# Kernel optimization log

Hardware: AMD Instinct MI355X
Metric: run time of the kernel (lower is better)

## Reference

```python
import jax, jax.numpy as jnp
import numpy as np

L, B, T, D, H, A, F, V, BIAS_DIM, E = 6, 16, 512, 512, 8, 64, 2048, 10000, 4, 200000
LN_EPS = 1e-3  # keras LayerNormalization default


def positional_encoding(d, max_len):
    pos = np.arange(max_len, dtype=np.float32)[:, None]
    i = np.arange(d, dtype=np.float32)[None, :]
    angle = pos / np.power(10000.0, (2.0 * np.floor(i / 2.0)) / d)
    pe = np.where((np.arange(d) % 2) == 0, np.sin(angle), np.cos(angle))
    return jnp.asarray(pe, jnp.float32)


def layer_norm(x, g, b):
    mu = jnp.mean(x, -1, keepdims=True)
    var = jnp.mean(jnp.square(x - mu), -1, keepdims=True)
    return (x - mu) * jax.lax.rsqrt(var + LN_EPS) * g + b


def attention(x, masks, bias_idx, Wq, Wk, Wv, Wo, be, bs):
    q = jnp.einsum('btd,dha->btha', x, Wq)
    k = jnp.einsum('btd,dha->btha', x, Wk)
    v = jnp.einsum('btd,dha->btha', x, Wv)
    alpha = jnp.einsum('bkha,bqha->bhqk', k, q)
    # sparse edge bias: scalar per edge = bias_embs[type] @ bias_scalar
    ev = (be[bias_idx[:, 0]] @ bs)[:, 0]                      # [E]
    dense = jnp.zeros((x.shape[0], x.shape[1], x.shape[1]), x.dtype)
    dense = dense.at[bias_idx[:, 1], bias_idx[:, 2], bias_idx[:, 3]].add(ev)  # scatter_nd semantics (add)
    ksum = jnp.sum(k, -1)                                     # [B,T,H]
    alpha = alpha + jnp.einsum('bqk,bkh->bhqk', dense, ksum)
    alpha = alpha * jax.lax.rsqrt(jnp.float32(A))
    alpha = alpha * masks + (1.0 - jnp.ceil(masks)) * jnp.finfo(jnp.float32).min
    alpha = jax.nn.softmax(alpha, -1)
    ctx = jnp.einsum('bhqk,bkha->bqha', alpha, v)
    return jnp.einsum('btha,had->btd', ctx, Wo)


def setup_inputs() -> dict:
    key = jax.random.key(0)
    ks = jax.random.split(key, 24)
    tokens = jax.random.randint(ks[0], (B, T), 0, V, dtype=jnp.int32)
    masks = jnp.ones((B, 1, T, T), jnp.float32)
    ab = jnp.stack([
        jax.random.randint(ks[1], (E,), 0, BIAS_DIM, dtype=jnp.int32),
        jax.random.randint(ks[2], (E,), 0, B, dtype=jnp.int32),
        jax.random.randint(ks[3], (E,), 0, T, dtype=jnp.int32),
        jax.random.randint(ks[4], (E,), 0, T, dtype=jnp.int32)], axis=1)
    s = 0.03
    return {
        'tokens': tokens, 'masks': masks, 'attention_bias': ab,
        'embed': jax.random.normal(ks[5], (V, D)) * (D ** -0.5),
        'Wq': jax.random.normal(ks[6], (L, D, H, A)) * s,
        'Wk': jax.random.normal(ks[7], (L, D, H, A)) * s,
        'Wv': jax.random.normal(ks[8], (L, D, H, A)) * s,
        'Wo': jax.random.normal(ks[9], (L, H, A, D)) * s,
        'be': jax.random.normal(ks[10], (L, BIAS_DIM, A)) * s,
        'bs': jax.random.normal(ks[11], (L, A, 1)) * s,
        'ln_g': jnp.ones((L, 2, D)), 'ln_b': jnp.zeros((L, 2, D)),
        'ff1_w': jax.random.normal(ks[12], (L, D, F)) * s,
        'ff1_b': jnp.zeros((L, F)),
        'ff2_w': jax.random.normal(ks[13], (L, F, D)) * s,
        'ff2_b': jnp.zeros((L, D)),
        'lnout_g': jnp.ones((D,)), 'lnout_b': jnp.zeros((D,)),
    }


def reference(tokens, masks, attention_bias, embed, Wq, Wk, Wv, Wo, be, bs,
              ln_g, ln_b, ff1_w, ff1_b, ff2_w, ff2_b, lnout_g, lnout_b):
    pos_enc = positional_encoding(D, 5000)
    x = embed[tokens] * jnp.sqrt(jnp.float32(D)) + pos_enc[:T]
    for l in range(L):
        h = layer_norm(x, ln_g[l, 0], ln_b[l, 0])
        x = x + attention(h, masks, attention_bias, Wq[l], Wk[l], Wv[l], Wo[l], be[l], bs[l])
        h = layer_norm(x, ln_g[l, 1], ln_b[l, 1])
        x = x + jax.nn.relu(h @ ff1_w[l] + ff1_b[l]) @ ff2_w[l] + ff2_b[l]
    return layer_norm(x, lnout_g, lnout_b)
```

## Files before the change

kernel.cpp:

```cpp
#include <hip/hip_runtime.h>
#include <hip/hip_bf16.h>

#define LNUM 6
#define BB 16
#define TT 512
#define DD 512
#define HH 8
#define AA 64
#define FFD 2048
#define EE 200000
#define BIASDIM 4
#define ATT_NEG (-3.402823466e38f)

typedef __bf16 bf16_t;
typedef __attribute__((ext_vector_type(8))) __bf16 bf16x8;
typedef __attribute__((ext_vector_type(4))) float f32x4;

typedef __attribute__((address_space(3))) void lds_void;
typedef const __attribute__((address_space(1))) void glb_void;

__device__ __forceinline__ void async_load16(const bf16_t* g, bf16_t* l) {
    __builtin_amdgcn_global_load_lds((glb_void*)g, (lds_void*)l, 16, 0, 0);
}

__global__ __launch_bounds__(256) void embed_pe_kernel(
    const int* __restrict__ tokens, const float* __restrict__ embed,
    float* __restrict__ x)
{
    int idx = blockIdx.x * 256 + threadIdx.x;
    int d  = idx & (DD - 1);
    int bt = idx >> 9;
    int t  = bt & (TT - 1);
    int tok = tokens[bt];
    float e = embed[(long long)tok * DD + d] * 22.62741699796952f;
    float p = (float)(2 * (d >> 1)) * (1.0f / (float)DD);
    float denom = exp2f(p * 13.287712379549449f);
    float angle = (float)t / denom;
    float pe = (d & 1) ? cosf(angle) : sinf(angle);
    x[idx] = e + pe;
}

template <typename TO>
__global__ __launch_bounds__(256) void ln_kernel(
    const float* __restrict__ x, TO* __restrict__ y,
    const float* __restrict__ g, const float* __restrict__ b)
{
    long long row = blockIdx.x;
    const float* xr = x + row * DD;
    int tid = threadIdx.x;
    float v0 = xr[tid], v1 = xr[tid + 256];
    float s = v0 + v1, sq = v0 * v0 + v1 * v1;
#pragma unroll
    for (int o = 32; o > 0; o >>= 1) {
        s  += __shfl_down(s, o);
        sq += __shfl_down(sq, o);
    }
    __shared__ float ss[4], sq4[4];
    if ((tid & 63) == 0) { ss[tid >> 6] = s; sq4[tid >> 6] = sq; }
    __syncthreads();
    float st  = ss[0] + ss[1] + ss[2] + ss[3];
    float sqt = sq4[0] + sq4[1] + sq4[2] + sq4[3];
    float mean = st * (1.0f / DD);
    float var  = sqt * (1.0f / DD) - mean * mean;
    float inv  = rsqrtf(var + 1e-3f);
    y[row * DD + tid]       = (TO)((v0 - mean) * inv * g[tid]       + b[tid]);
    y[row * DD + tid + 256] = (TO)((v1 - mean) * inv * g[tid + 256] + b[tid + 256]);
}

template <typename TO, int S>
__global__ __launch_bounds__(256) void reduce_ln_kernel(
    float* __restrict__ x, const float* __restrict__ P,
    TO* __restrict__ y, const float* __restrict__ g, const float* __restrict__ b)
{
    const long long NXc = (long long)BB * TT * DD;
    long long row = blockIdx.x;
    int tid = threadIdx.x;
    long long i0 = row * DD + tid;
    float v0 = x[i0], v1 = x[i0 + 256];
#pragma unroll
    for (int s = 0; s < S; s++) {
        v0 += P[(long long)s * NXc + i0];
        v1 += P[(long long)s * NXc + i0 + 256];
    }
    x[i0] = v0; x[i0 + 256] = v1;
    float s2 = v0 + v1, sq = v0 * v0 + v1 * v1;
#pragma unroll
    for (int o = 32; o > 0; o >>= 1) {
        s2 += __shfl_down(s2, o);
        sq += __shfl_down(sq, o);
    }
    __shared__ float ss[4], sq4[4];
    if ((tid & 63) == 0) { ss[tid >> 6] = s2; sq4[tid >> 6] = sq; }
    __syncthreads();
    float st  = ss[0] + ss[1] + ss[2] + ss[3];
    float sqt = sq4[0] + sq4[1] + sq4[2] + sq4[3];
    float mean = st * (1.0f / DD);
    float var  = sqt * (1.0f / DD) - mean * mean;
    float inv  = rsqrtf(var + 1e-3f);
    y[i0]       = (TO)((v0 - mean) * inv * g[tid]       + b[tid]);
    y[i0 + 256] = (TO)((v1 - mean) * inv * g[tid + 256] + b[tid + 256]);
}

__global__ __launch_bounds__(256) void ksum_kernel(
    const bf16_t* __restrict__ k, float* __restrict__ ks)
{
    int idx = blockIdx.x * 256 + threadIdx.x;
    long long base = (long long)idx * AA;
    float s = 0.f;
#pragma unroll
    for (int a = 0; a < AA; a++) s += (float)k[base + a];
    ks[idx] = s;
}

__global__ __launch_bounds__(256) void cnt_scatter_kernel(
    const int* __restrict__ ab, unsigned int* __restrict__ cm)
{
    int e = blockIdx.x * 256 + threadIdx.x;
    if (e < EE) {
        int ty = ab[e * 4 + 0];
        int b  = ab[e * 4 + 1];
        int q  = ab[e * 4 + 2];
        int kk = ab[e * 4 + 3];
        atomicAdd(&cm[((long long)b * TT + q) * TT + kk], 1u << (4 * ty));
    }
}

__global__ __launch_bounds__(256) void cm_mask_kernel(
    unsigned int* __restrict__ cm, const float* __restrict__ masks)
{
    long long i = ((long long)blockIdx.x * 256 + threadIdx.x) * 4;
    uint4 c = *(const uint4*)(cm + i);
    f32x4 m = *(const f32x4*)(masks + i);
    c.x = (__float_as_uint(m[0]) & 0xffff0000u) | (c.x & 0xffffu);
    c.y = (__float_as_uint(m[1]) & 0xffff0000u) | (c.y & 0xffffu);
    c.z = (__float_as_uint(m[2]) & 0xffff0000u) | (c.z & 0xffffu);
    c.w = (__float_as_uint(m[3]) & 0xffff0000u) | (c.w & 0xffffu);
    *(uint4*)(cm + i) = c;
}

__global__ __launch_bounds__(256) void wconv_kernel(
    const float* __restrict__ in, bf16_t* __restrict__ out, int R, int Cc)
{
    __shared__ bf16_t tile[64][65];
    int c0 = blockIdx.x * 64, r0 = blockIdx.y * 64;
    int tid = threadIdx.x;
#pragma unroll
    for (int i = 0; i < 16; i++) {
        int idx = tid + i * 256; int r = idx >> 6, c = idx & 63;
        tile[c][r] = (bf16_t)in[(long long)(r0 + r) * Cc + c0 + c];
    }
    __syncthreads();
#pragma unroll
    for (int i = 0; i < 16; i++) {
        int idx = tid + i * 256; int rr = idx >> 6, cc = idx & 63;
        out[(long long)(c0 + rr) * R + r0 + cc] = tile[rr][cc];
    }
}

struct Ptr4 { const float* p[4]; };

__global__ __launch_bounds__(256) void wconv4_kernel(Ptr4 srcs, bf16_t* __restrict__ out)
{
    __shared__ bf16_t tile[64][65];
    int z = blockIdx.z;
    const float* in = srcs.p[z];
    bf16_t* o = out + (long long)z * DD * DD;
    int c0 = blockIdx.x * 64, r0 = blockIdx.y * 64;
    int tid = threadIdx.x;
#pragma unroll
    for (int i = 0; i < 16; i++) {
        int idx = tid + i * 256; int r = idx >> 6, c = idx & 63;
        tile[c][r] = (bf16_t)in[(long long)(r0 + r) * DD + c0 + c];
    }
    __syncthreads();
#pragma unroll
    for (int i = 0; i < 16; i++) {
        int idx = tid + i * 256; int rr = idx >> 6, cc = idx & 63;
        o[(long long)(c0 + rr) * DD + r0 + cc] = tile[rr][cc];
    }
}

__global__ __launch_bounds__(256) void vtrans_kernel(
    const bf16_t* __restrict__ v, bf16_t* __restrict__ vT)
{
    __shared__ bf16_t tile[64][65];
    int bh = blockIdx.y; int b = bh >> 3, h = bh & 7;
    int t0 = blockIdx.x * 64;
    int tid = threadIdx.x;
#pragma unroll
    for (int i = 0; i < 16; i++) {
        int idx = tid + i * 256; int r = idx >> 6, c = idx & 63;
        tile[c][r] = v[((long long)(b * TT + t0 + r) * HH + h) * AA + c];
    }
    __syncthreads();
#pragma unroll
    for (int i = 0; i < 16; i++) {
        int idx = tid + i * 256; int a = idx >> 6, t2 = idx & 63;
        vT[(((long long)b * HH + h) * AA + a) * TT + t0 + t2] = tile[a][t2];
    }
}

__global__ __launch_bounds__(256) void fused_attn_kernel(
    const bf16_t* __restrict__ qg, const bf16_t* __restrict__ kg,
    const bf16_t* __restrict__ vT, const unsigned int* __restrict__ cm,
    const float* __restrict__ ksum, const float* __restrict__ be_l,
    const float* __restrict__ bs_l, bf16_t* __restrict__ ctx)
{
    __shared__ __align__(16) bf16_t Ks[64 * 64];
    __shared__ __align__(16) bf16_t Vs[64 * 64];
    __shared__ __align__(16) bf16_t Plds[4 * 16 * 88];
    __shared__ float evs[BIASDIM];

    int tid = threadIdx.x;
    int wave = tid >> 6, lane = tid & 63;
    int row16 = lane & 15, quad = lane >> 4;
    int bid = blockIdx.x;
    int bh = bid & 127; int b = bh >> 3, h = bh & 7;
    int qw = (bid >> 7) * 64 + wave * 16;

    if (wave == 0) {
        float bsv = bs_l[lane];
#pragma unroll
        for (int t = 0; t < BIASDIM; t++) {
            float p = be_l[t * AA + lane] * bsv;
#pragma unroll
            for (int off = 32; off > 0; off >>= 1) p += __shfl_xor(p, off);
            if (lane == 0) evs[t] = p;
        }
    }

    bf16x8 qf[2];
    {
        const bf16_t* qp = qg + (((long long)b * TT + qw + row16) * HH + h) * AA + quad * 8;
        qf[0] = *(const bf16x8*)(qp);
        qf[1] = *(const bf16x8*)(qp + 32);
    }

    f32x4 o[4] = {};
    float m_r[4], l_r[4];
#pragma unroll
    for (int r = 0; r < 4; r++) { m_r[r] = -3.0e38f; l_r[r] = 0.f; }

    bf16_t* Pw = Plds + wave * 16 * 88;
    const unsigned int* cmbase = cm + (long long)b * TT * TT;
    const float* ksbase = ksum + (long long)b * TT * HH + h;

    for (int kt = 0; kt < 8; kt++) {
        int t0 = kt * 64;

        unsigned int cmw[4][4];
        float ksv4[4];
#pragma unroll
        for (int n = 0; n < 4; n++) {
            int ktok = t0 + n * 16 + row16;
            ksv4[n] = ksbase[(long long)ktok * HH];
#pragma unroll
            for (int r = 0; r < 4; r++)
                cmw[n][r] = cmbase[(long long)(qw + quad * 4 + r) * TT + ktok];
        }

#pragma unroll
        for (int p = tid; p < 512; p += 256) {
            int r = p >> 3, s = p & 7, c = s ^ (r & 7);
            async_load16(kg + (((long long)b * TT + t0 + r) * HH + h) * AA + c * 8,
                         Ks + p * 8);
        }
#pragma unroll
        for (int p = tid; p < 512; p += 256) {
            int r = p >> 3, s = p & 7, c = s ^ (r & 7);
            async_load16(vT + ((long long)bh * AA + r) * TT + t0 + c * 8,
                         Vs + p * 8);
        }
        __syncthreads();

        f32x4 s4[4] = {};
        __builtin_amdgcn_s_setprio(1);
#pragma unroll
        for (int n = 0; n < 4; n++) {
            int row = n * 16 + row16;
            int sw = row & 7;
            bf16x8 kf0 = *(const bf16x8*)(Ks + row * 64 + ((quad ^ sw) * 8));
            bf16x8 kf1 = *(const bf16x8*)(Ks + row * 64 + (((quad + 4) ^ sw) * 8));
            s4[n] = __builtin_amdgcn_mfma_f32_16x16x32_bf16(qf[0], kf0, s4[n], 0, 0, 0);
            s4[n] = __builtin_amdgcn_mfma_f32_16x16x32_bf16(qf[1], kf1, s4[n], 0, 0, 0);
        }
        __builtin_amdgcn_s_setprio(0);

        float e0 = evs[0], e1 = evs[1], e2 = evs[2], e3 = evs[3];
        float val[4][4];
#pragma unroll
        for (int n = 0; n < 4; n++) {
#pragma unroll
            for (int r = 0; r < 4; r++) {
                unsigned int w = cmw[n][r];
                float mk = __uint_as_float(w & 0xffff0000u);
                float d = e0 * (float)(w & 15u)
                        + e1 * (float)((w >> 4) & 15u)
                        + e2 * (float)((w >> 8) & 15u)
                        + e3 * (float)((w >> 12) & 15u);
                float vv = 0.125f * fmaf(d, ksv4[n], s4[n][r]);
                val[n][r] = (mk == 0.f) ? ATT_NEG : vv * mk;
            }
        }

        float scl[4];
#pragma unroll
        for (int r = 0; r < 4; r++) {
            float mx = fmaxf(fmaxf(val[0][r], val[1][r]), fmaxf(val[2][r], val[3][r]));
#pragma unroll
            for (int off = 1; off < 16; off <<= 1) mx = fmaxf(mx, __shfl_xor(mx, off));
            float mnew = fmaxf(m_r[r], mx);
            float sc = __expf(m_r[r] - mnew);
            float ps = 0.f;
#pragma unroll
            for (int n = 0; n < 4; n++) {
                float p = __expf(val[n][r] - mnew);
                val[n][r] = p;
                ps += p;
            }
#pragma unroll
            for (int off = 1; off < 16; off <<= 1) ps += __shfl_xor(ps, off);
            l_r[r] = l_r[r] * sc + ps;
            m_r[r] = mnew;
            scl[r] = sc;
        }
#pragma unroll
        for (int j = 0; j < 4; j++)
#pragma unroll
            for (int r = 0; r < 4; r++) o[j][r] *= scl[r];

#pragma unroll
        for (int n = 0; n < 4; n++)
#pragma unroll
            for (int r = 0; r < 4; r++)
                Pw[(quad * 4 + r) * 88 + n * 16 + row16] = (bf16_t)val[n][r];
        asm volatile("s_waitcnt lgkmcnt(0)" ::: "memory");

        bf16x8 pa0 = *(const bf16x8*)(Pw + row16 * 88 + quad * 8);
        bf16x8 pa1 = *(const bf16x8*)(Pw + row16 * 88 + 32 + quad * 8);
        __builtin_amdgcn_s_setprio(1);
#pragma unroll
        for (int j = 0; j < 4; j++) {
            int row = j * 16 + row16;
            int sw = row & 7;
            bf16x8 vb0 = *(const bf16x8*)(Vs + row * 64 + ((quad ^ sw) * 8));
            bf16x8 vb1 = *(const bf16x8*)(Vs + row * 64 + (((quad + 4) ^ sw) * 8));
            o[j] = __builtin_amdgcn_mfma_f32_16x16x32_bf16(pa0, vb0, o[j], 0, 0, 0);
            o[j] = __builtin_amdgcn_mfma_f32_16x16x32_bf16(pa1, vb1, o[j], 0, 0, 0);
        }
        __builtin_amdgcn_s_setprio(0);
        __syncthreads();
    }

#pragma unroll
    for (int r = 0; r < 4; r++) {
        float invl = 1.0f / l_r[r];
        int qgl = qw + quad * 4 + r;
        bf16_t* cp = ctx + (((long long)b * TT + qgl) * HH + h) * AA;
#pragma unroll
        for (int j = 0; j < 4; j++)
            cp[j * 16 + row16] = (bf16_t)(o[j][r] * invl);
    }
}

#define PSTAGE(kc0, slot)                                                     \
    {                                                                         \
        bf16_t* At = sm + (slot) * 16384;                                     \
        bf16_t* Bt = At + 8192;                                               \
        _Pragma("unroll")                                                     \
        for (int i = 0; i < 4; i++) {                                         \
            int qq = tid + i * 256;                                           \
            int r = qq >> 3, ck = qq & 7;                                     \
            int cc = (kc0) + ((ck ^ (r & 7)) * 8);                            \
            async_load16(Ag + (long long)(m0 + r) * lda + cc, At + qq * 8);   \
            async_load16(Bg + (long long)(n0 + r) * ldb + cc, Bt + qq * 8);   \
        }                                                                     \
    }

#define PLOAD()                                                               \
    _Pragma("unroll")                                                         \
    for (int mf = 0; mf < 4; mf++) {                                          \
        int ra = wm * 64 + mf * 16 + row16;                                   \
        _Pragma("unroll")                                                     \
        for (int ks2 = 0; ks2 < 2; ks2++)                                     \
            a8[mf][ks2] = *(const bf16x8*)(Ac + ra * 64 +                     \
                              (((ks2 * 4 + quad) ^ (ra & 7)) * 8));           \
    }                                                                         \
    _Pragma("unroll")                                                         \
    for (int nf = 0; nf < 4; nf++) {                                          \
        int rb = wn * 64 + nf * 16 + row16;                                   \
        _Pragma("unroll")                                                     \
        for (int ks2 = 0; ks2 < 2; ks2++)                                     \
            b8[nf][ks2] = *(const bf16x8*)(Bc + rb * 64 +                     \
                              (((ks2 * 4 + quad) ^ (rb & 7)) * 8));           \
    }

#define PMM()                                                                 \
    _Pragma("unroll")                                                         \
    for (int mf = 0; mf < 4; mf++)                                            \
        _Pragma("unroll")                                                     \
        for (int nf = 0; nf < 4; nf++)                                        \
            _Pragma("unroll")                                                 \
            for (int ks2 = 0; ks2 < 2; ks2++)                                 \
                acc[mf][nf] = __builtin_amdgcn_mfma_f32_16x16x32_bf16(        \
                    a8[mf][ks2], b8[nf][ks2], acc[mf][nf], 0, 0, 0);

#define PIPE_BODY(KBEG, NT)                                                   \
    PSTAGE((KBEG), 0);                                                        \
    int c = 0;                                                                \
    for (int t = 0; t < (NT); ++t, c ^= 1) {                                  \
        if (t + 1 < (NT)) {                                                   \
            PSTAGE((KBEG) + (t + 1) * 64, c ^ 1);                             \
            asm volatile("s_waitcnt vmcnt(8)" ::: "memory");                  \
        } else {                                                              \
            asm volatile("s_waitcnt vmcnt(0)" ::: "memory");                  \
        }                                                                     \
        __builtin_amdgcn_sched_barrier(0);                                    \
        __builtin_amdgcn_s_barrier();                                         \
        __builtin_amdgcn_sched_barrier(0);                                    \
        const bf16_t* Ac = sm + c * 16384;                                    \
        const bf16_t* Bc = Ac + 8192;                                         \
        bf16x8 a8[4][2], b8[4][2];                                            \
        PLOAD();                                                              \
        asm volatile("s_waitcnt lgkmcnt(0)" ::: "memory");                    \
        __builtin_amdgcn_sched_barrier(0);                                    \
        __builtin_amdgcn_s_barrier();                                        \
        __builtin_amdgcn_sched_barrier(0);                                    \
        __builtin_amdgcn_s_setprio(1);                                        \
        PMM();                                                                \
        __builtin_amdgcn_s_setprio(0);                                        \
    }

template <typename TC, int ACCUM, int RELU>
__global__ __launch_bounds__(256, 2) void gemm_pipe(
    const bf16_t* __restrict__ Ag, const bf16_t* __restrict__ Bg, TC* __restrict__ Cg,
    int K, int lda, int ldb, int ldc,
    long long sAz, long long sBz, long long sCz,
    const float* __restrict__ bias)
{
    extern __shared__ __align__(16) bf16_t sm[];
    int z = blockIdx.z;
    Ag += z * sAz; Bg += z * sBz; Cg += z * sCz;

    int tid = threadIdx.x;
    int wave = tid >> 6, lane = tid & 63;
    int wm = wave >> 1, wn = wave & 1;
    int row16 = lane & 15, quad = lane >> 4;
    int m0 = blockIdx.x * 128, n0 = blockIdx.y * 128;

    f32x4 acc[4][4] = {};
    int nt = K >> 6;
    PIPE_BODY(0, nt);

#pragma unroll
    for (int mf = 0; mf < 4; mf++) {
#pragma unroll
        for (int nf = 0; nf < 4; nf++) {
#pragma unroll
            for (int r = 0; r < 4; r++) {
                int m = m0 + wm * 64 + mf * 16 + quad * 4 + r;
                int n = n0 + wn * 64 + nf * 16 + row16;
                float vv = acc[mf][nf][r];
                if (bias) vv += bias[n];
                if (ACCUM) vv += (float)Cg[(long long)m * ldc + n];
                if (RELU) vv = fmaxf(vv, 0.f);
                Cg[(long long)m * ldc + n] = (TC)vv;
            }
        }
    }
}

template <int SPLIT>
__global__ __launch_bounds__(256, 2) void gemm_pipe_splitk(
    const bf16_t* __restrict__ Ag, const bf16_t* __restrict__ Bg,
    float* __restrict__ Cg, float* __restrict__ Pg,
    int K, int lda, int ldb, int ldc, const float* __restrict__ bias)
{
    extern __shared__ __align__(16) bf16_t sm[];
    int z = blockIdx.z;
    int kbeg = z * (K / SPLIT);

    int tid = threadIdx.x;
    int wave = tid >> 6, lane = tid & 63;
    int wm = wave >> 1, wn = wave & 1;
    int row16 = lane & 15, quad = lane >> 4;
    int m0 = blockIdx.x * 128, n0 = blockIdx.y * 128;

    f32x4 acc[4][4] = {};
    int nt = (K / SPLIT) >> 6;
    PIPE_BODY(kbeg, nt);

    const long long NXc = (long long)BB * TT * DD;
#pragma unroll
    for (int mf = 0; mf < 4; mf++) {
#pragma unroll
        for (int nf = 0; nf < 4; nf++) {
#pragma unroll
            for (int r = 0; r < 4; r++) {
                int m = m0 + wm * 64 + mf * 16 + quad * 4 + r;
                int n = n0 + wn * 64 + nf * 16 + row16;
                float vv = acc[mf][nf][r];
                long long ci = (long long)m * ldc + n;
                if (z == 0) {
                    if (bias) vv += bias[n];
                    Cg[ci] = Cg[ci] + vv;
                } else {
                    Pg[(long long)(z - 1) * NXc + ci] = vv;
                }
            }
        }
    }
}

extern "C" void kernel_launch(void* const* d_in, const int* in_sizes, int n_in,
                              void* d_out, int out_size, void* d_ws, size_t ws_size,
                              hipStream_t stream)
{
    const int*   tokens = (const int*)d_in[0];
    const float* masks  = (const float*)d_in[1];
    const int*   ab     = (const int*)d_in[2];
    const float* embed  = (const float*)d_in[3];
    const float* Wq     = (const float*)d_in[4];
    const float* Wk     = (const float*)d_in[5];
    const float* Wv     = (const float*)d_in[6];
    const float* Wo     = (const float*)d_in[7];
    const float* be     = (const float*)d_in[8];
    const float* bs     = (const float*)d_in[9];
    const float* ln_g   = (const float*)d_in[10];
    const float* ln_b   = (const float*)d_in[11];
    const float* ff1w   = (const float*)d_in[12];
    const float* ff1b   = (const float*)d_in[13];
    const float* ff2w   = (const float*)d_in[14];
    const float* ff2b   = (const float*)d_in[15];
    const float* lng    = (const float*)d_in[16];
    const float* lnb    = (const float*)d_in[17];
    float* out = (float*)d_out;

    const long long NX = (long long)BB * TT * DD;
    float* x     = (float*)d_ws;
    float* ks    = x + NX;
    bf16_t* h_bf = (bf16_t*)(ks + (long long)BB * TT * HH);
    unsigned int* cm = (unsigned int*)(h_bf + NX);
    bf16_t* q    = (bf16_t*)(cm + NX);
    bf16_t* k    = q + NX;
    bf16_t* v    = k + NX;
    bf16_t* vT   = v + NX;
    bf16_t* wqT  = vT + NX;
    bf16_t* wkT  = wqT + (long long)DD * DD;
    bf16_t* wvT  = wkT + (long long)DD * DD;
    bf16_t* woT  = wvT + (long long)DD * DD;
    bf16_t* ff1T = woT + (long long)DD * DD;
    bf16_t* ff2T = ff1T + (long long)DD * FFD;
    bf16_t* ffm  = ff2T + (long long)FFD * DD;

    float* partFF  = (float*)q;
    float* partCtx = (float*)v;

    const size_t LDSP = 65536;

    embed_pe_kernel<<<dim3(NX / 256), dim3(256), 0, stream>>>(tokens, embed, x);

    hipMemsetAsync(cm, 0, sizeof(unsigned int) * (size_t)NX, stream);
    cnt_scatter_kernel<<<dim3((EE + 255) / 256), dim3(256), 0, stream>>>(ab, cm);
    cm_mask_kernel<<<dim3((int)(NX / 1024)), dim3(256), 0, stream>>>(cm, masks);

    for (int l = 0; l < LNUM; l++) {
        if (l == 0) {
            ln_kernel<bf16_t><<<dim3(BB * TT), dim3(256), 0, stream>>>(
                x, h_bf, ln_g + (l * 2 + 0) * DD, ln_b + (l * 2 + 0) * DD);
        } else {
            reduce_ln_kernel<bf16_t, 1><<<dim3(BB * TT), dim3(256), 0, stream>>>(
                x, partFF, h_bf, ln_g + (l * 2 + 0) * DD, ln_b + (l * 2 + 0) * DD);
        }

        Ptr4 p4;
        p4.p[0] = Wq + (long long)l * DD * HH * AA;
        p4.p[1] = Wk + (long long)l * DD * HH * AA;
        p4.p[2] = Wv + (long long)l * DD * HH * AA;
        p4.p[3] = Wo + (long long)l * HH * AA * DD;
        wconv4_kernel<<<dim3(8, 8, 4), dim3(256), 0, stream>>>(p4, wqT);
        wconv_kernel<<<dim3(FFD / 64, DD / 64, 1), dim3(256), 0, stream>>>(
            ff1w + (long long)l * DD * FFD, ff1T, DD, FFD);
        wconv_kernel<<<dim3(DD / 64, FFD / 64, 1), dim3(256), 0, stream>>>(
            ff2w + (long long)l * FFD * DD, ff2T, FFD, DD);

        const float* ff1b_l = ff1b + (long long)l * FFD;
        const float* ff2b_l = ff2b + (long long)l * DD;

        gemm_pipe<bf16_t, 0, 0><<<dim3(64, 4, 3), dim3(256), LDSP, stream>>>(
            h_bf, wqT, q, 512, 512, 512, 512,
            0LL, (long long)DD * DD, NX, nullptr);

        vtrans_kernel<<<dim3(8, BB * HH), dim3(256), 0, stream>>>(v, vT);
        ksum_kernel<<<dim3(BB * TT * HH / 256), dim3(256), 0, stream>>>(k, ks);

        fused_attn_kernel<<<dim3((TT / 64) * BB * HH), dim3(256), 0, stream>>>(
            q, k, vT, cm, ks,
            be + (long long)l * BIASDIM * AA, bs + (long long)l * AA, h_bf);

        gemm_pipe_splitk<2><<<dim3(64, 4, 2), dim3(256), LDSP, stream>>>(
            h_bf, woT, x, partCtx, 512, 512, 512, 512, nullptr);

        reduce_ln_kernel<bf16_t, 1><<<dim3(BB * TT), dim3(256), 0, stream>>>(
            x, partCtx, h_bf, ln_g + (l * 2 + 1) * DD, ln_b + (l * 2 + 1) * DD);

        gemm_pipe<bf16_t, 0, 1><<<dim3(64, 16, 1), dim3(256), LDSP, stream>>>(
            h_bf, ff1T, ffm, 512, 512, 512, 2048, 0LL, 0LL, 0LL, ff1b_l);

        gemm_pipe_splitk<2><<<dim3(64, 4, 2), dim3(256), LDSP, stream>>>(
            ffm, ff2T, x, partFF, 2048, 2048, 2048, 512, ff2b_l);
    }

    reduce_ln_kernel<float, 1><<<dim3(BB * TT), dim3(256), 0, stream>>>(
        x, partFF, out, lng, lnb);
}
```

Baseline: 1.533 ms.

## Use 256x256-tile 512-thread GEMM for fused QKV and FF1 projections

Adds a gemm256 kernel with 256x256 output tiles, 8 waves and a double-buffered 128KB LDS pipeline that interleaves half-K stage loads with MFMA groups. It replaces the 128x128 gemm_pipe for the QKV projection, which now runs as one N=1536 GEMM with outputs routed to q/k/v by column, and for the FF1 GEMM with bias and ReLU. The larger tiles raise arithmetic intensity and cut redundant global loads. In exchange, the QKV launch has only 192 blocks and FF1 only 256 on a 256-CU part, with heavy register and LDS use per block, so occupancy drops.

```diff
diff --git a/kernel.cpp b/kernel.cpp
--- a/kernel.cpp
+++ b/kernel.cpp
@@ -360,6 +360,129 @@
 #pragma unroll
         for (int j = 0; j < 4; j++)
             cp[j * 16 + row16] = (bf16_t)(o[j][r] * invl);
+    }
+}
+
+#define S256(Gb, ld, rb, kc0, so)                                             \
+    _Pragma("unroll")                                                         \
+    for (int i5 = 0; i5 < 2; i5++) {                                          \
+        int s5 = tid + i5 * 512;                                              \
+        int j5 = s5 >> 3, cp5 = s5 & 7, cl5 = cp5 ^ (j5 & 7);                 \
+        async_load16((Gb) + (long long)((rb) + 2 * j5 + (cl5 >> 2)) * (ld)    \
+                         + (kc0) + (cl5 & 3) * 8,                             \
+                     sm + (so) + s5 * 8);                                     \
+    }
+
+#define LDA256(bo, ks, mg)                                                    \
+    _Pragma("unroll")                                                         \
+    for (int mf = 0; mf < 4; mf++) {                                          \
+        int ra = wm * 128 + ((mg) * 4 + mf) * 16 + row16;                     \
+        int j5 = ra >> 1;                                                     \
+        int cl5 = ((ra & 1) * 4 + quad) ^ (j5 & 7);                           \
+        a8[mf] = *(const bf16x8*)(sm + (bo) + (ks) * 8192 + j5 * 64 + cl5 * 8);\
+    }
+
+#define LDB256(bo, ks)                                                        \
+    _Pragma("unroll")                                                         \
+    for (int nf = 0; nf < 4; nf++) {                                          \
+        int rb2 = wn * 64 + nf * 16 + row16;                                  \
+        int j5 = rb2 >> 1;                                                    \
+        int cl5 = ((rb2 & 1) * 4 + quad) ^ (j5 & 7);                          \
+        b8[nf] = *(const bf16x8*)(sm + (bo) + 16384 + (ks) * 8192             \
+                                  + j5 * 64 + cl5 * 8);                       \
+    }
+
+#define MM256(mg)                                                             \
+    _Pragma("unroll")                                                         \
+    for (int mf = 0; mf < 4; mf++)                                            \
+        _Pragma("unroll")                                                     \
+        for (int nf = 0; nf < 4; nf++)                                        \
+            acc[(mg) * 4 + mf][nf] = __builtin_amdgcn_mfma_f32_16x16x32_bf16( \
+                a8[mf], b8[nf], acc[(mg) * 4 + mf][nf], 0, 0, 0);
+
+template <typename TC, int RELU, int QKVC>
+__global__ __launch_bounds__(512, 2) void gemm256(
+    const bf16_t* __restrict__ Ag, const bf16_t* __restrict__ Bg,
+    TC* __restrict__ Cg, int K, int lda, int ldb, int ldc,
+    long long sCz, const float* __restrict__ bias)
+{
+    extern __shared__ __align__(16) bf16_t sm[];
+    int tid = threadIdx.x;
+    int wave = tid >> 6, lane = tid & 63;
+    int wm = wave >> 2, wn = wave & 3;
+    int row16 = lane & 15, quad = lane >> 4;
+    int m0 = blockIdx.x * 256, n0 = blockIdx.y * 256;
+
+    f32x4 acc[8][4] = {};
+    int nt = K >> 6;
+
+    S256(Ag, lda, m0, 0, 0);
+    S256(Bg, ldb, n0, 0, 16384);
+    S256(Ag, lda, m0, 32, 8192);
+    S256(Bg, ldb, n0, 32, 16384 + 8192);
+
+    for (int t = 0; t < nt; ++t) {
+        int bo = (t & 1) * 32768;
+        int bs = 32768 - bo;
+        int kn = (t + 1) * 64;
+        bf16x8 a8[4], b8[4];
+        if (t + 1 < nt) {
+            S256(Ag, lda, m0, kn, bs);
+            asm volatile("s_waitcnt vmcnt(6)" ::: "memory");
+        } else {
+            asm volatile("s_waitcnt vmcnt(4)" ::: "memory");
+        }
+        __builtin_amdgcn_sched_barrier(0);
+        __builtin_amdgcn_s_barrier();
+        __builtin_amdgcn_sched_barrier(0);
+        LDA256(bo, 0, 0); LDB256(bo, 0);
+        asm volatile("s_waitcnt lgkmcnt(0)" ::: "memory");
+        __builtin_amdgcn_sched_barrier(0);
+        __builtin_amdgcn_s_setprio(1); MM256(0); __builtin_amdgcn_s_setprio(0);
+        if (t + 1 < nt) S256(Bg, ldb, n0, kn, bs + 16384);
+        LDA256(bo, 0, 1);
+        asm volatile("s_waitcnt lgkmcnt(0)" ::: "memory");
+        __builtin_amdgcn_sched_barrier(0);
+        __builtin_amdgcn_s_setprio(1); MM256(1); __builtin_amdgcn_s_setprio(0);
+        if (t + 1 < nt) {
+            S256(Ag, lda, m0, kn + 32, bs + 8192);
+            asm volatile("s_waitcnt vmcnt(6)" ::: "memory");
+        } else {
+            asm volatile("s_waitcnt vmcnt(0)" ::: "memory");
+        }
+        __builtin_amdgcn_sched_barrier(0);
+        __builtin_amdgcn_s_barrier();
+        __builtin_amdgcn_sched_barrier(0);
+        LDA256(bo, 1, 0); LDB256(bo, 1);
+        asm volatile("s_waitcnt lgkmcnt(0)" ::: "memory");
+        __builtin_amdgcn_sched_barrier(0);
+        __builtin_amdgcn_s_setprio(1); MM256(0); __builtin_amdgcn_s_setprio(0);
+        if (t + 1 < nt) S256(Bg, ldb, n0, kn + 32, bs + 16384 + 8192);
+        LDA256(bo, 1, 1);
+        asm volatile("s_waitcnt lgkmcnt(0)" ::: "memory");
+        __builtin_amdgcn_sched_barrier(0);
+        __builtin_amdgcn_s_setprio(1); MM256(1); __builtin_amdgcn_s_setprio(0);
+    }
+
+#pragma unroll
+    for (int mf2 = 0; mf2 < 8; mf2++) {
+#pragma unroll
+        for (int nf2 = 0; nf2 < 4; nf2++) {
+#pragma unroll
+            for (int r = 0; r < 4; r++) {
+                int m  = m0 + wm * 128 + mf2 * 16 + quad * 4 + r;
+                int ng = n0 + wn * 64 + nf2 * 16 + row16;
+                float vv = acc[mf2][nf2][r];
+                if (bias) vv += bias[ng];
+                if (RELU) vv = fmaxf(vv, 0.f);
+                if (QKVC) {
+                    TC* Cb = Cg + (long long)(ng >> 9) * sCz;
+                    Cb[(long long)m * ldc + (ng & 511)] = (TC)vv;
+                } else {
+                    Cg[(long long)m * ldc + ng] = (TC)vv;
+                }
+            }
+        }
     }
 }
 
@@ -431,45 +554,6 @@
         __builtin_amdgcn_s_setprio(0);                                        \
     }
 
-template <typename TC, int ACCUM, int RELU>
-__global__ __launch_bounds__(256, 2) void gemm_pipe(
-    const bf16_t* __restrict__ Ag, const bf16_t* __restrict__ Bg, TC* __restrict__ Cg,
-    int K, int lda, int ldb, int ldc,
-    long long sAz, long long sBz, long long sCz,
-    const float* __restrict__ bias)
-{
-    extern __shared__ __align__(16) bf16_t sm[];
-    int z = blockIdx.z;
-    Ag += z * sAz; Bg += z * sBz; Cg += z * sCz;
-
-    int tid = threadIdx.x;
-    int wave = tid >> 6, lane = tid & 63;
-    int wm = wave >> 1, wn = wave & 1;
-    int row16 = lane & 15, quad = lane >> 4;
-    int m0 = blockIdx.x * 128, n0 = blockIdx.y * 128;
-
-    f32x4 acc[4][4] = {};
-    int nt = K >> 6;
-    PIPE_BODY(0, nt);
-
-#pragma unroll
-    for (int mf = 0; mf < 4; mf++) {
-#pragma unroll
-        for (int nf = 0; nf < 4; nf++) {
-#pragma unroll
-            for (int r = 0; r < 4; r++) {
-                int m = m0 + wm * 64 + mf * 16 + quad * 4 + r;
-                int n = n0 + wn * 64 + nf * 16 + row16;
-                float vv = acc[mf][nf][r];
-                if (bias) vv += bias[n];
-                if (ACCUM) vv += (float)Cg[(long long)m * ldc + n];
-                if (RELU) vv = fmaxf(vv, 0.f);
-                Cg[(long long)m * ldc + n] = (TC)vv;
-            }
-        }
-    }
-}
-
 template <int SPLIT>
 __global__ __launch_bounds__(256, 2) void gemm_pipe_splitk(
     const bf16_t* __restrict__ Ag, const bf16_t* __restrict__ Bg,
@@ -557,6 +641,7 @@
     float* partCtx = (float*)v;
 
     const size_t LDSP = 65536;
+    const size_t LDS8 = 131072;
 
     embed_pe_kernel<<<dim3(NX / 256), dim3(256), 0, stream>>>(tokens, embed, x);
 
@@ -587,9 +672,8 @@
         const float* ff1b_l = ff1b + (long long)l * FFD;
         const float* ff2b_l = ff2b + (long long)l * DD;
 
-        gemm_pipe<bf16_t, 0, 0><<<dim3(64, 4, 3), dim3(256), LDSP, stream>>>(
-            h_bf, wqT, q, 512, 512, 512, 512,
-            0LL, (long long)DD * DD, NX, nullptr);
+        gemm256<bf16_t, 0, 1><<<dim3(32, 6), dim3(512), LDS8, stream>>>(
+            h_bf, wqT, q, 512, 512, 512, 512, NX, nullptr);
 
         vtrans_kernel<<<dim3(8, BB * HH), dim3(256), 0, stream>>>(v, vT);
         ksum_kernel<<<dim3(BB * TT * HH / 256), dim3(256), 0, stream>>>(k, ks);
@@ -604,8 +688,8 @@
         reduce_ln_kernel<bf16_t, 1><<<dim3(BB * TT), dim3(256), 0, stream>>>(
             x, partCtx, h_bf, ln_g + (l * 2 + 1) * DD, ln_b + (l * 2 + 1) * DD);
 
-        gemm_pipe<bf16_t, 0, 1><<<dim3(64, 16, 1), dim3(256), LDSP, stream>>>(
-            h_bf, ff1T, ffm, 512, 512, 512, 2048, 0LL, 0LL, 0LL, ff1b_l);
+        gemm256<bf16_t, 1, 0><<<dim3(32, 8), dim3(512), LDS8, stream>>>(
+            h_bf, ff1T, ffm, 512, 512, 512, 2048, 0LL, ff1b_l);
 
         gemm_pipe_splitk<2><<<dim3(64, 4, 2), dim3(256), LDSP, stream>>>(
             ffm, ff2T, x, partFF, 2048, 2048, 2048, 512, ff2b_l);
```

Result: faster. 1.474 ms (-3.9%).
